# Optimization experiments

Hardware: AMD Instinct MI355X
Metric: run time of the kernel (lower is better)

Reference implementation:

```python
import jax, jax.numpy as jnp
import numpy as np

DIM = 2048
N_HEADS = 32
N_KV_HEADS = 8
HEAD_DIM = 64
REPEATS = N_HEADS // N_KV_HEADS
SLIDING_WINDOW = 1024
EPS = 1e-6
B, T = 2, 2048


def _alibi_slopes(n):
    # n_heads=32 is a power of 2
    r = 2.0 ** (-8.0 / n)
    return jnp.asarray([r ** i for i in range(n)], dtype=jnp.float32)


def _rms_norm(x, w, eps):
    # RMSNorm over the last (flattened heads*head_dim) axis
    var = jnp.mean(x * x, axis=-1, keepdims=True)
    return x * jax.lax.rsqrt(var + eps) * w


def setup_inputs() -> dict:
    key = jax.random.key(0)
    ks = jax.random.split(key, 6)
    s = 0.02
    return {
        "x": jax.random.normal(ks[0], (B, T, DIM), jnp.float32),
        "wq": jax.random.normal(ks[1], (N_HEADS * HEAD_DIM, DIM), jnp.float32) * s,
        "wk": jax.random.normal(ks[2], (N_KV_HEADS * HEAD_DIM, DIM), jnp.float32) * s,
        "wv": jax.random.normal(ks[3], (N_KV_HEADS * HEAD_DIM, DIM), jnp.float32) * s,
        "wo": jax.random.normal(ks[4], (DIM, N_HEADS * HEAD_DIM), jnp.float32) * s,
        "q_norm_w": jnp.ones((N_HEADS * HEAD_DIM,), jnp.float32),
        "k_norm_w": jnp.ones((N_KV_HEADS * HEAD_DIM,), jnp.float32),
    }


def reference(x, wq, wk, wv, wo, q_norm_w, k_norm_w):
    bsz, seqlen, _ = x.shape
    xq = _rms_norm(x @ wq.T, q_norm_w, EPS)
    xk = _rms_norm(x @ wk.T, k_norm_w, EPS)
    xv = x @ wv.T
    xq = xq.reshape(bsz, seqlen, N_HEADS, HEAD_DIM).transpose(0, 2, 1, 3)  # b h t d
    xk = xk.reshape(bsz, seqlen, N_KV_HEADS, HEAD_DIM).transpose(0, 2, 1, 3)
    xv = xv.reshape(bsz, seqlen, N_KV_HEADS, HEAD_DIM).transpose(0, 2, 1, 3)
    # GQA: repeat_interleave kv heads
    xk = jnp.repeat(xk, REPEATS, axis=1)
    xv = jnp.repeat(xv, REPEATS, axis=1)

    pos = jnp.arange(seqlen)
    dist = pos[None, :] - pos[:, None]                     # [t,s] = s - t (<=0 on causal side)
    slopes = _alibi_slopes(N_HEADS)
    alibi = slopes[:, None, None] * dist.astype(jnp.float32)  # [h,t,s]
    allowed = (dist <= 0) & (dist >= -SLIDING_WINDOW)      # causal + sliding window
    bias = jnp.where(allowed[None], alibi, -jnp.inf)       # [h,t,s]

    scale = 1.0 / jnp.sqrt(jnp.asarray(HEAD_DIM, jnp.float32))
    scores = jnp.einsum("bhtd,bhsd->bhts", xq, xk) * scale + bias[None]
    attn = jax.nn.softmax(scores, axis=-1)
    out = jnp.einsum("bhts,bhsd->bhtd", attn, xv)          # [b,h,t,d]
    out = out.transpose(0, 2, 1, 3).reshape(bsz, seqlen, N_HEADS * HEAD_DIM)
    return out @ wo.T
```

## Files before the change

kernel.cpp:

```cpp
#include <hip/hip_runtime.h>


typedef _Float16 f16;
typedef __attribute__((ext_vector_type(8))) _Float16 f16x8;
typedef __attribute__((ext_vector_type(4))) _Float16 f16x4;
typedef __attribute__((ext_vector_type(2))) _Float16 f16x2;
typedef __attribute__((ext_vector_type(4))) float f32x4;

#define T_ 2048
#define NH 32
#define NKV 8
#define HD 64
#define WINDOW 1024
#define EPS_ 1e-6f
#define LOG2E 1.44269504088896340736f
#define LDQKV 3072

__device__ inline void async16(void* lds, const void* g) {
  __builtin_amdgcn_global_load_lds(
      (const __attribute__((address_space(1))) unsigned int*)g,
      (__attribute__((address_space(3))) unsigned int*)lds, 16, 0, 0);
}

struct CvtArgs {
  const float* src[5];
  f16* dst[5];
  int n4[5];
};
__global__ __launch_bounds__(256) void cvt_multi(CvtArgs a) {
  const int seg = blockIdx.y;
  const float* in = a.src[seg];
  f16* out = a.dst[seg];
  const int n4 = a.n4[seg];
  for (int i = blockIdx.x * blockDim.x + threadIdx.x; i < n4;
       i += gridDim.x * blockDim.x) {
    float4 v = ((const float4*)in)[i];
    f16x4 o;
    o[0] = (f16)v.x; o[1] = (f16)v.y; o[2] = (f16)v.z; o[3] = (f16)v.w;
    ((f16x4*)out)[i] = o;
  }
}

#define DSRD(p, off) (*(const f16x8*)((p) + (off)))

__global__ __launch_bounds__(512, 1) void gemm_nt192(const f16* __restrict__ A,
                                                     const f16* __restrict__ B,
                                                     f16* __restrict__ C) {
  constexpr int K = 2048, ldc = 3072;
  extern __shared__ char smem[];
  f16* sA = (f16*)smem;
  f16* sB = (f16*)(smem + 65536);

  const int gx = gridDim.x;
  const int nwg = gx * gridDim.y;
  int bid = blockIdx.y * gx + blockIdx.x;
  bid = (bid & 7) * (nwg >> 3) + (bid >> 3);
  const int m0 = (bid / gx) * 256;
  const int n0 = (bid % gx) * 192;

  const int tid = threadIdx.x;
  const int lane = tid & 63;
  const int wave = tid >> 6;
  const int quad = lane >> 4, l16 = lane & 15;
  const int wm = wave >> 2, wn = wave & 3;

  const int srow = tid >> 3;
  const int sgr = (((tid & 7) ^ (srow & 7))) * 8;
  const f16* gA = A + (size_t)(m0 + srow) * K + sgr;
  const f16* gB = B + (size_t)(n0 + srow) * K + sgr;
  const size_t r64 = (size_t)64 * K;

  const char* cA = (const char*)sA;
  const char* cB = (const char*)sB;
  const int xm = (l16 & 7) << 4;
  const int xk0 = (quad * 16) ^ xm;
  const int xk1 = (64 + quad * 16) ^ xm;
  const int abase = (wm * 128 + l16) * 128;
  const int bbase = (wn * 48 + l16) * 128;

  f32x4 acc[8][3] = {};
  const int nt = K >> 6;

#pragma unroll
  for (int a = 0; a < 4; ++a)
    async16(sA + a * 4096 + tid * 8, gA + (size_t)a * r64);
#pragma unroll
  for (int rb = 0; rb < 3; ++rb)
    async16(sB + rb * 4096 + tid * 8, gB + (size_t)rb * r64);
  asm volatile("s_waitcnt vmcnt(0)" ::: "memory");
  __builtin_amdgcn_s_barrier();

  for (int t = 0; t < nt; ++t) {
    const int bufoA = (t & 1) << 15;
    const int bufoB = (t & 1) * 24576;
    f16* sAn = sA + (((t & 1) ^ 1) << 14);
    f16* sBn = sB + ((t & 1) ^ 1) * 12288;
    const bool st = (t + 1 < nt);
    const size_t gk = (size_t)(t + 1) * 64;

    f16x8 af[4], bf[3][2];

    auto ldA = [&](int mh, int xk) {
#pragma unroll
      for (int i = 0; i < 4; ++i)
        af[i] = DSRD(cA, bufoA + abase + mh * 8192 + i * 2048 + xk);
    };
    auto mm = [&](int mh, int kc) {
      __builtin_amdgcn_s_barrier();
      asm volatile("s_waitcnt lgkmcnt(0)" ::: "memory");
      __builtin_amdgcn_sched_barrier(0);
      __builtin_amdgcn_s_setprio(1);
#pragma unroll
      for (int i = 0; i < 4; ++i)
#pragma unroll
        for (int j = 0; j < 3; ++j)
          acc[mh * 4 + i][j] = __builtin_amdgcn_mfma_f32_16x16x32_f16(
              af[i], bf[j][kc], acc[mh * 4 + i][j], 0, 0, 0);
      __builtin_amdgcn_s_setprio(0);
    };

    ldA(0, xk0);
#pragma unroll
    for (int j = 0; j < 3; ++j) {
      bf[j][0] = DSRD(cB, bufoB + bbase + j * 2048 + xk0);
      bf[j][1] = DSRD(cB, bufoB + bbase + j * 2048 + xk1);
    }
    if (st) {
#pragma unroll
      for (int a = 0; a < 4; ++a)
        async16(sAn + a * 4096 + tid * 8, gA + a * r64 + gk);
    }
    mm(0, 0);
    __builtin_amdgcn_s_barrier();

    ldA(0, xk1);
    if (st) {
#pragma unroll
      for (int rb = 0; rb < 3; ++rb)
        async16(sBn + rb * 4096 + tid * 8, gB + rb * r64 + gk);
    }
    mm(0, 1);
    __builtin_amdgcn_s_barrier();

    ldA(1, xk0);
    mm(1, 0);
    __builtin_amdgcn_s_barrier();

    ldA(1, xk1);
    mm(1, 1);
    if (st) asm volatile("s_waitcnt vmcnt(0)" ::: "memory");
    __builtin_amdgcn_s_barrier();
  }

#pragma unroll
  for (int im = 0; im < 8; ++im) {
    const int row0 = m0 + wm * 128 + im * 16 + quad * 4;
#pragma unroll
    for (int j = 0; j < 3; ++j) {
      const int col = n0 + wn * 48 + j * 16 + l16;
#pragma unroll
      for (int r = 0; r < 4; ++r)
        C[(size_t)(row0 + r) * ldc + col] = (f16)acc[im][j][r];
    }
  }
}

template <int BN>
__global__ __launch_bounds__(512, 2) void gemm_nt8(const f16* __restrict__ A,
                                                   const f16* __restrict__ B,
                                                   void* __restrict__ C,
                                                   int M, int N, int K, int ldc,
                                                   int out_f32) {
  constexpr int WN = BN / 4;
  constexpr int JN = WN / 32;
  constexpr int RB = BN / 64;
  constexpr int BUFB = BN * 128;
  extern __shared__ char smem[];
  f16* sA = (f16*)smem;
  f16* sB = (f16*)(smem + 65536);

  const int gx = gridDim.x;
  const int nwg = gx * gridDim.y;
  int bid = blockIdx.y * gx + blockIdx.x;
  if (!(nwg & 7)) bid = (bid & 7) * (nwg >> 3) + (bid >> 3);
  const int m0 = (bid / gx) * 256;
  const int n0 = (bid % gx) * BN;

  const int tid = threadIdx.x;
  const int lane = tid & 63;
  const int wave = tid >> 6;
  const int quad = lane >> 4, l16 = lane & 15;
  const int wm = wave >> 2, wn = wave & 3;

  const int srow = tid >> 3;
  const int sgr = (((tid & 7) ^ (srow & 7))) * 8;
  const f16* gA = A + (size_t)(m0 + srow) * K + sgr;
  const f16* gB = B + (size_t)(n0 + srow) * K + sgr;
  const size_t r64 = (size_t)64 * K;

  const char* cA = (const char*)sA;
  const char* cB = (const char*)sB;
  const int xm = (l16 & 7) << 4;
  const int xk0 = (quad * 16) ^ xm;
  const int xk1 = (64 + quad * 16) ^ xm;
  const int abase = (wm * 128 + l16) * 128;
  const int bbase = (wn * WN + l16) * 128;

  f32x4 acc[8][2 * JN] = {};
  const int nt = K >> 6;

#pragma unroll
  for (int a = 0; a < 4; ++a)
    async16(sA + a * 4096 + tid * 8, gA + (size_t)a * r64);
#pragma unroll
  for (int rb = 0; rb < RB; ++rb)
    async16(sB + rb * 4096 + tid * 8, gB + (size_t)rb * r64);
  asm volatile("s_waitcnt vmcnt(0)" ::: "memory");
  __builtin_amdgcn_s_barrier();

  for (int t = 0; t < nt; ++t) {
    const int bufoA = (t & 1) << 15;
    const int bufoB = (t & 1) * BUFB;
    f16* sAn = sA + (((t & 1) ^ 1) << 14);
    f16* sBn = sB + ((t & 1) ^ 1) * (BUFB / 2);
    const bool st = (t + 1 < nt);
    const size_t gk = (size_t)(t + 1) * 64;

    f16x8 af[4][2], bf[JN][2];

    auto ldA = [&](int mh) {
#pragma unroll
      for (int i = 0; i < 4; ++i) {
        af[i][0] = DSRD(cA, bufoA + abase + mh * 8192 + i * 2048 + xk0);
        af[i][1] = DSRD(cA, bufoA + abase + mh * 8192 + i * 2048 + xk1);
      }
    };
    auto ldB = [&](int nh) {
#pragma unroll
      for (int j = 0; j < JN; ++j) {
        bf[j][0] = DSRD(cB, bufoB + bbase + nh * (WN / 2) * 128 + j * 2048 + xk0);
        bf[j][1] = DSRD(cB, bufoB + bbase + nh * (WN / 2) * 128 + j * 2048 + xk1);
      }
    };
    auto mm = [&](int mh, int nh) {
      __builtin_amdgcn_s_barrier();
      asm volatile("s_waitcnt lgkmcnt(0)" ::: "memory");
      __builtin_amdgcn_sched_barrier(0);
      __builtin_amdgcn_s_setprio(1);
#pragma unroll
      for (int i = 0; i < 4; ++i) {
#pragma unroll
        for (int j = 0; j < JN; ++j) {
          acc[mh * 4 + i][nh * JN + j] = __builtin_amdgcn_mfma_f32_16x16x32_f16(
              af[i][0], bf[j][0], acc[mh * 4 + i][nh * JN + j], 0, 0, 0);
          acc[mh * 4 + i][nh * JN + j] = __builtin_amdgcn_mfma_f32_16x16x32_f16(
              af[i][1], bf[j][1], acc[mh * 4 + i][nh * JN + j], 0, 0, 0);
        }
      }
      __builtin_amdgcn_s_setprio(0);
    };

    ldA(0); ldB(0);
    if (st) {
#pragma unroll
      for (int a = 0; a < 4; ++a)
        async16(sAn + a * 4096 + tid * 8, gA + a * r64 + gk);
#pragma unroll
      for (int rb = 0; rb < RB; ++rb)
        async16(sBn + rb * 4096 + tid * 8, gB + rb * r64 + gk);
    }
    mm(0, 0);
    __builtin_amdgcn_s_barrier();

    ldB(1);
    mm(0, 1);
    __builtin_amdgcn_s_barrier();

    ldA(1); ldB(0);
    mm(1, 0);
    __builtin_amdgcn_s_barrier();

    ldB(1);
    mm(1, 1);
    if (st) asm volatile("s_waitcnt vmcnt(0)" ::: "memory");
    __builtin_amdgcn_s_barrier();
  }

#pragma unroll
  for (int im = 0; im < 8; ++im) {
    const int row0 = m0 + wm * 128 + im * 16 + quad * 4;
#pragma unroll
    for (int jn = 0; jn < 2 * JN; ++jn) {
      const int col = n0 + wn * WN + jn * 16 + l16;
#pragma unroll
      for (int r = 0; r < 4; ++r) {
        const float v = acc[im][jn][r];
        if (out_f32) ((float*)C)[(size_t)(row0 + r) * ldc + col] = v;
        else         ((f16*)C)[(size_t)(row0 + r) * ldc + col] = (f16)v;
      }
    }
  }
}

__global__ __launch_bounds__(256) void rmsnorm2(f16* __restrict__ xqkv,
                                                const float* __restrict__ qw,
                                                const float* __restrict__ kw) {
  __shared__ float red[4];
  const int which = blockIdx.y;
  const int tid = threadIdx.x;

  auto block_sum = [&](float ss) -> float {
#pragma unroll
    for (int off = 32; off > 0; off >>= 1) ss += __shfl_down(ss, off);
    if ((tid & 63) == 0) red[tid >> 6] = ss;
    __syncthreads();
    return red[0] + red[1] + red[2] + red[3];
  };

  if (which == 0) {
    f16* p = xqkv + (size_t)blockIdx.x * LDQKV;
    f16x8 v = ((const f16x8*)p)[tid];
    float f[8];
    float ss = 0.f;
#pragma unroll
    for (int j = 0; j < 8; ++j) { f[j] = (float)v[j]; ss += f[j] * f[j]; }
    const float scale = rsqrtf(block_sum(ss) / 2048.0f + EPS_);
    const float4 w0 = ((const float4*)qw)[tid * 2];
    const float4 w1 = ((const float4*)qw)[tid * 2 + 1];
    f16x8 o;
    o[0] = (f16)(f[0] * scale * w0.x); o[1] = (f16)(f[1] * scale * w0.y);
    o[2] = (f16)(f[2] * scale * w0.z); o[3] = (f16)(f[3] * scale * w0.w);
    o[4] = (f16)(f[4] * scale * w1.x); o[5] = (f16)(f[5] * scale * w1.y);
    o[6] = (f16)(f[6] * scale * w1.z); o[7] = (f16)(f[7] * scale * w1.w);
    ((f16x8*)p)[tid] = o;
  } else {
    f16* p = xqkv + (size_t)blockIdx.x * LDQKV + 2048;
    f16x2 v = ((const f16x2*)p)[tid];
    const float f0 = (float)v[0], f1 = (float)v[1];
    const float scale = rsqrtf(block_sum(f0 * f0 + f1 * f1) / 512.0f + EPS_);
    const float2 w = ((const float2*)kw)[tid];
    f16x2 o;
    o[0] = (f16)(f0 * scale * w.x);
    o[1] = (f16)(f1 * scale * w.y);
    ((f16x2*)p)[tid] = o;
  }
}

__global__ __launch_bounds__(256) void kvfrag(const f16* __restrict__ xqkv,
                                              f16* __restrict__ Kf,
                                              f16* __restrict__ Vf) {
  __shared__ f16 Lk[64][72];
  __shared__ f16 Lv[64][72];
  const int kt = blockIdx.x;
  const int b = blockIdx.y >> 3, kh = blockIdx.y & 7;
  const int t0 = kt * 64;
  const int tid = threadIdx.x;
  const int r = tid >> 3, c = (tid & 7) * 8;
#pragma unroll
  for (int rp = 0; rp < 2; ++rp) {
    const int rr = r + rp * 32;
    const f16* src = xqkv + (size_t)(b * T_ + t0 + rr) * LDQKV + kh * 64 + c;
    *(f16x8*)(&Lk[rr][c]) = *(const f16x8*)(src + 2048);
    *(f16x8*)(&Lv[rr][c]) = *(const f16x8*)(src + 2560);
  }
  __syncthreads();
  const size_t obase = ((size_t)(b * 8 + kh) * 32 + kt) * 4096;
#pragma unroll
  for (int cc0 = 0; cc0 < 2; ++cc0) {
    const int cc = tid + cc0 * 256;
    const int nb = cc >> 7, kc = (cc >> 6) & 1, ln = cc & 63;
    const int qd = ln >> 4, s16 = ln & 15;
    *(f16x8*)(Kf + obase + cc * 8) = *(const f16x8*)(&Lk[nb * 16 + s16][kc * 32 + qd * 8]);
    f16x8 o;
#pragma unroll
    for (int j = 0; j < 8; ++j) o[j] = Lv[kc * 32 + qd * 8 + j][nb * 16 + s16];
    *(f16x8*)(Vf + obase + cc * 8) = o;
  }
}

__global__ __launch_bounds__(256, 8) void attn(const f16* __restrict__ Q,
                                               const f16* __restrict__ Kf,
                                               const f16* __restrict__ Vf,
                                               f16* __restrict__ O) {
  constexpr int LDW = 72;
  __shared__ f16 Qs[64 * LDW];
  __shared__ float Lx[4][16];

  const int qt = 31 - blockIdx.x;
  const int h = blockIdx.y, b = blockIdx.z;
  const int kh = h >> 2;
  const int q0 = qt * 64;
  const int tid = threadIdx.x;
  const int lane = tid & 63, wave = tid >> 6;
  const int quad = lane >> 4, l16 = lane & 15;
  const float scale2 = 0.125f * LOG2E;
  const float slope2 = exp2f(-0.25f * (float)h) * LOG2E;
  const float M2 = 10.0f;

  const int sr = tid >> 3, sc = (tid & 7) * 8;

#pragma unroll
  for (int rp = 0; rp < 2; ++rp) {
    const int rr = sr + rp * 32;
    *(f16x8*)(Qs + rr * LDW + sc) =
        *(const f16x8*)(Q + (size_t)(b * T_ + q0 + rr) * LDQKV + h * HD + sc);
  }
  __syncthreads();
  f16x8 qf[2];
#pragma unroll
  for (int kc = 0; kc < 2; ++kc)
    qf[kc] = *(const f16x8*)(Qs + (wave * 16 + l16) * LDW + kc * 32 + quad * 8);
  f16* Ps = Qs + wave * 16 * LDW;

  f32x4 o_acc[4] = {};
  float lsum = 0.f;

  const int kt_lo = (q0 >= WINDOW) ? ((q0 - WINDOW) >> 6) : 0;
  const int my_q = q0 + wave * 16 + l16;
  const f16* kfb = Kf + (size_t)(b * 8 + kh) * 131072 + lane * 8;
  const f16* vfb = Vf + (size_t)(b * 8 + kh) * 131072 + lane * 8;

  float sr4[4];
#pragma unroll
  for (int r = 0; r < 4; ++r) sr4[r] = slope2 * (float)r;
  float base = slope2 * (float)(kt_lo * 64 + quad * 4 - my_q) - M2;
  const float bstep = slope2 * 64.0f;
  const float b16 = slope2 * 16.0f;

  for (int kt = kt_lo; kt <= qt; ++kt) {
    const int k0 = kt * 64;
    const f16* kp = kfb + kt * 4096;
    const f16* vp = vfb + kt * 4096;
    const bool maskt = (kt == qt) || (q0 + 63 - k0 > WINDOW);

    float bnb = base;
#pragma unroll
    for (int nb = 0; nb < 4; ++nb) {
      f32x4 a = {0.f, 0.f, 0.f, 0.f};
#pragma unroll
      for (int kc = 0; kc < 2; ++kc) {
        const f16x8 kfr = *(const f16x8*)(kp + (nb * 2 + kc) * 512);
        a = __builtin_amdgcn_mfma_f32_16x16x32_f16(kfr, qf[kc], a, 0, 0, 0);
      }
      f16x4 pk;
#pragma unroll
      for (int r = 0; r < 4; ++r) {
        float v = fmaf(a[r], scale2, bnb + sr4[r]);
        if (maskt) {
          const int dist = k0 + nb * 16 + quad * 4 + r - my_q;
          if (dist > 0 || dist < -WINDOW) v = -1e30f;
        }
        const float p = __builtin_amdgcn_exp2f(v);
        lsum += p;
        pk[r] = (f16)p;
      }
      *(f16x4*)(Ps + l16 * LDW + nb * 16 + quad * 4) = pk;
      bnb += b16;
    }
    base += bstep;

#pragma unroll
    for (int nb = 0; nb < 4; ++nb) {
#pragma unroll
      for (int kc = 0; kc < 2; ++kc) {
        const f16x8 pa = *(const f16x8*)(Ps + l16 * LDW + kc * 32 + quad * 8);
        const f16x8 vb = *(const f16x8*)(vp + (nb * 2 + kc) * 512);
        o_acc[nb] = __builtin_amdgcn_mfma_f32_16x16x32_f16(pa, vb, o_acc[nb], 0, 0, 0);
      }
    }
  }

  lsum += __shfl_xor(lsum, 16);
  lsum += __shfl_xor(lsum, 32);
  if (quad == 0) Lx[wave][l16] = lsum;
  float rl[4];
#pragma unroll
  for (int r = 0; r < 4; ++r) rl[r] = 1.0f / Lx[wave][quad * 4 + r];

#pragma unroll
  for (int r = 0; r < 4; ++r) {
    const int q = q0 + wave * 16 + quad * 4 + r;
#pragma unroll
    for (int nb = 0; nb < 4; ++nb)
      O[(size_t)(b * T_ + q) * (NH * HD) + h * HD + nb * 16 + l16] =
          (f16)(o_acc[nb][r] * rl[r]);
  }
}

extern "C" void kernel_launch(void* const* d_in, const int* in_sizes, int n_in,
                              void* d_out, int out_size, void* d_ws, size_t ws_size,
                              hipStream_t stream) {
  const float* x  = (const float*)d_in[0];
  const float* wq = (const float*)d_in[1];
  const float* wk = (const float*)d_in[2];
  const float* wv = (const float*)d_in[3];
  const float* wo = (const float*)d_in[4];
  const float* qw = (const float*)d_in[5];
  const float* kw = (const float*)d_in[6];
  float* out = (float*)d_out;

  char* ws = (char*)d_ws;
  size_t off = 0;
  auto carve = [&](size_t bytes) -> char* {
    char* p = ws + off;
    off += (bytes + 255) & ~(size_t)255;
    return p;
  };
  f16* xh    = (f16*)carve((size_t)4096 * 2048 * 2);
  f16* wqkvh = (f16*)carve((size_t)3072 * 2048 * 2);
  f16* woh   = (f16*)carve((size_t)2048 * 2048 * 2);
  f16* xqkv  = (f16*)carve((size_t)4096 * 3072 * 2);
  f16* Kf = wqkvh;
  f16* Vf = wqkvh + (size_t)16 * 131072;
  f16* ao = xh;

  static bool attr_done = false;
  if (!attr_done) {
    (void)hipFuncSetAttribute((const void*)gemm_nt192,
                              hipFuncAttributeMaxDynamicSharedMemorySize,
                              114688);
    (void)hipFuncSetAttribute((const void*)gemm_nt8<128>,
                              hipFuncAttributeMaxDynamicSharedMemorySize,
                              98304);
    attr_done = true;
  }

  CvtArgs ca;
  ca.src[0] = x;  ca.dst[0] = xh;                            ca.n4[0] = (4096 * 2048) / 4;
  ca.src[1] = wq; ca.dst[1] = wqkvh;                         ca.n4[1] = (2048 * 2048) / 4;
  ca.src[2] = wk; ca.dst[2] = wqkvh + (size_t)2048 * 2048;   ca.n4[2] = (512 * 2048) / 4;
  ca.src[3] = wv; ca.dst[3] = wqkvh + (size_t)2560 * 2048;   ca.n4[3] = (512 * 2048) / 4;
  ca.src[4] = wo; ca.dst[4] = woh;                           ca.n4[4] = (2048 * 2048) / 4;
  cvt_multi<<<dim3(1024, 5), 256, 0, stream>>>(ca);

  gemm_nt192<<<dim3(16, 16), 512, 114688, stream>>>(xh, wqkvh, xqkv);
  rmsnorm2<<<dim3(4096, 2), 256, 0, stream>>>(xqkv, qw, kw);
  kvfrag<<<dim3(32, 16), 256, 0, stream>>>(xqkv, Kf, Vf);
  attn<<<dim3(32, 32, 2), 256, 0, stream>>>(xqkv, Kf, Vf, ao);
  gemm_nt8<128><<<dim3(16, 16), 512, 98304, stream>>>(ao, woh, out, 4096, 2048, 2048, 2048, 1);
}
```

Measured before the change: 305.7 us.

## Process 128 query rows per attention block to reuse K/V fragments

Each attention block now covers 128 query rows instead of 64, with each wave handling two 16-row sub-tiles that share every loaded K and V fragment. The aim is to halve the global K/V fragment traffic and the number of loads per MFMA. In exchange, register use per thread rises, launch bounds drop to 4 blocks per SM, the grid is half as large, and the tile spans more fully-masked key columns at the causal and window edges.

```diff
diff --git a/kernel.cpp b/kernel.cpp
--- a/kernel.cpp
+++ b/kernel.cpp
@@ -378,18 +378,18 @@
   }
 }
 
-__global__ __launch_bounds__(256, 8) void attn(const f16* __restrict__ Q,
+__global__ __launch_bounds__(256, 4) void attn(const f16* __restrict__ Q,
                                                const f16* __restrict__ Kf,
                                                const f16* __restrict__ Vf,
                                                f16* __restrict__ O) {
   constexpr int LDW = 72;
-  __shared__ f16 Qs[64 * LDW];
-  __shared__ float Lx[4][16];
-
-  const int qt = 31 - blockIdx.x;
+  __shared__ f16 Qs[128 * LDW];
+  __shared__ float Lx[4][2][16];
+
+  const int qt2 = 15 - blockIdx.x;
   const int h = blockIdx.y, b = blockIdx.z;
   const int kh = h >> 2;
-  const int q0 = qt * 64;
+  const int q0 = qt2 * 128;
   const int tid = threadIdx.x;
   const int lane = tid & 63, wave = tid >> 6;
   const int quad = lane >> 4, l16 = lane & 15;
@@ -400,90 +400,124 @@
   const int sr = tid >> 3, sc = (tid & 7) * 8;
 
 #pragma unroll
-  for (int rp = 0; rp < 2; ++rp) {
+  for (int rp = 0; rp < 4; ++rp) {
     const int rr = sr + rp * 32;
     *(f16x8*)(Qs + rr * LDW + sc) =
         *(const f16x8*)(Q + (size_t)(b * T_ + q0 + rr) * LDQKV + h * HD + sc);
   }
   __syncthreads();
-  f16x8 qf[2];
-#pragma unroll
-  for (int kc = 0; kc < 2; ++kc)
-    qf[kc] = *(const f16x8*)(Qs + (wave * 16 + l16) * LDW + kc * 32 + quad * 8);
-  f16* Ps = Qs + wave * 16 * LDW;
-
-  f32x4 o_acc[4] = {};
-  float lsum = 0.f;
+  f16x8 qa[2], qb[2];
+#pragma unroll
+  for (int kc = 0; kc < 2; ++kc) {
+    qa[kc] = *(const f16x8*)(Qs + (wave * 32 + l16) * LDW + kc * 32 + quad * 8);
+    qb[kc] = *(const f16x8*)(Qs + (wave * 32 + 16 + l16) * LDW + kc * 32 + quad * 8);
+  }
+  f16* PsA = Qs + (wave * 32) * LDW;
+  f16* PsB = Qs + (wave * 32 + 16) * LDW;
+
+  f32x4 o0[4] = {}, o1[4] = {};
+  float lsA = 0.f, lsB = 0.f;
 
   const int kt_lo = (q0 >= WINDOW) ? ((q0 - WINDOW) >> 6) : 0;
-  const int my_q = q0 + wave * 16 + l16;
+  const int kt_hi = (q0 + 127) >> 6;
+  const int gA0 = q0 + wave * 32;
+  const int gB0 = gA0 + 16;
+  const int qA = gA0 + l16;
+  const int qB = qA + 16;
   const f16* kfb = Kf + (size_t)(b * 8 + kh) * 131072 + lane * 8;
   const f16* vfb = Vf + (size_t)(b * 8 + kh) * 131072 + lane * 8;
 
   float sr4[4];
 #pragma unroll
   for (int r = 0; r < 4; ++r) sr4[r] = slope2 * (float)r;
-  float base = slope2 * (float)(kt_lo * 64 + quad * 4 - my_q) - M2;
+  float baseA = slope2 * (float)(kt_lo * 64 + quad * 4 - qA) - M2;
+  float baseB = slope2 * (float)(kt_lo * 64 + quad * 4 - qB) - M2;
   const float bstep = slope2 * 64.0f;
   const float b16 = slope2 * 16.0f;
 
-  for (int kt = kt_lo; kt <= qt; ++kt) {
+  for (int kt = kt_lo; kt <= kt_hi; ++kt) {
     const int k0 = kt * 64;
     const f16* kp = kfb + kt * 4096;
     const f16* vp = vfb + kt * 4096;
-    const bool maskt = (kt == qt) || (q0 + 63 - k0 > WINDOW);
-
-    float bnb = base;
+    const bool maskA = (k0 + 63 > gA0) || (k0 + WINDOW < gA0 + 15);
+    const bool maskB = (k0 + 63 > gB0) || (k0 + WINDOW < gB0 + 15);
+
+    float bnbA = baseA, bnbB = baseB;
 #pragma unroll
     for (int nb = 0; nb < 4; ++nb) {
+      const f16x8 k0f = *(const f16x8*)(kp + (nb * 2) * 512);
+      const f16x8 k1f = *(const f16x8*)(kp + (nb * 2 + 1) * 512);
       f32x4 a = {0.f, 0.f, 0.f, 0.f};
-#pragma unroll
-      for (int kc = 0; kc < 2; ++kc) {
-        const f16x8 kfr = *(const f16x8*)(kp + (nb * 2 + kc) * 512);
-        a = __builtin_amdgcn_mfma_f32_16x16x32_f16(kfr, qf[kc], a, 0, 0, 0);
+      a = __builtin_amdgcn_mfma_f32_16x16x32_f16(k0f, qa[0], a, 0, 0, 0);
+      a = __builtin_amdgcn_mfma_f32_16x16x32_f16(k1f, qa[1], a, 0, 0, 0);
+      f32x4 c = {0.f, 0.f, 0.f, 0.f};
+      c = __builtin_amdgcn_mfma_f32_16x16x32_f16(k0f, qb[0], c, 0, 0, 0);
+      c = __builtin_amdgcn_mfma_f32_16x16x32_f16(k1f, qb[1], c, 0, 0, 0);
+
+      f16x4 pkA, pkB;
+#pragma unroll
+      for (int r = 0; r < 4; ++r) {
+        const int key = k0 + nb * 16 + quad * 4 + r;
+        float vA = fmaf(a[r], scale2, bnbA + sr4[r]);
+        if (maskA) {
+          const int dist = key - qA;
+          if (dist > 0 || dist < -WINDOW) vA = -1e30f;
+        }
+        const float pA = __builtin_amdgcn_exp2f(vA);
+        lsA += pA;
+        pkA[r] = (f16)pA;
+        float vB = fmaf(c[r], scale2, bnbB + sr4[r]);
+        if (maskB) {
+          const int dist = key - qB;
+          if (dist > 0 || dist < -WINDOW) vB = -1e30f;
+        }
+        const float pB = __builtin_amdgcn_exp2f(vB);
+        lsB += pB;
+        pkB[r] = (f16)pB;
       }
-      f16x4 pk;
-#pragma unroll
-      for (int r = 0; r < 4; ++r) {
-        float v = fmaf(a[r], scale2, bnb + sr4[r]);
-        if (maskt) {
-          const int dist = k0 + nb * 16 + quad * 4 + r - my_q;
-          if (dist > 0 || dist < -WINDOW) v = -1e30f;
-        }
-        const float p = __builtin_amdgcn_exp2f(v);
-        lsum += p;
-        pk[r] = (f16)p;
-      }
-      *(f16x4*)(Ps + l16 * LDW + nb * 16 + quad * 4) = pk;
-      bnb += b16;
-    }
-    base += bstep;
-
+      *(f16x4*)(PsA + l16 * LDW + nb * 16 + quad * 4) = pkA;
+      *(f16x4*)(PsB + l16 * LDW + nb * 16 + quad * 4) = pkB;
+      bnbA += b16; bnbB += b16;
+    }
+    baseA += bstep; baseB += bstep;
+
+    const f16x8 paA0 = *(const f16x8*)(PsA + l16 * LDW + quad * 8);
+    const f16x8 paA1 = *(const f16x8*)(PsA + l16 * LDW + 32 + quad * 8);
+    const f16x8 paB0 = *(const f16x8*)(PsB + l16 * LDW + quad * 8);
+    const f16x8 paB1 = *(const f16x8*)(PsB + l16 * LDW + 32 + quad * 8);
 #pragma unroll
     for (int nb = 0; nb < 4; ++nb) {
-#pragma unroll
-      for (int kc = 0; kc < 2; ++kc) {
-        const f16x8 pa = *(const f16x8*)(Ps + l16 * LDW + kc * 32 + quad * 8);
-        const f16x8 vb = *(const f16x8*)(vp + (nb * 2 + kc) * 512);
-        o_acc[nb] = __builtin_amdgcn_mfma_f32_16x16x32_f16(pa, vb, o_acc[nb], 0, 0, 0);
-      }
-    }
-  }
-
-  lsum += __shfl_xor(lsum, 16);
-  lsum += __shfl_xor(lsum, 32);
-  if (quad == 0) Lx[wave][l16] = lsum;
-  float rl[4];
-#pragma unroll
-  for (int r = 0; r < 4; ++r) rl[r] = 1.0f / Lx[wave][quad * 4 + r];
-
+      const f16x8 v0 = *(const f16x8*)(vp + (nb * 2) * 512);
+      const f16x8 v1 = *(const f16x8*)(vp + (nb * 2 + 1) * 512);
+      o0[nb] = __builtin_amdgcn_mfma_f32_16x16x32_f16(paA0, v0, o0[nb], 0, 0, 0);
+      o0[nb] = __builtin_amdgcn_mfma_f32_16x16x32_f16(paA1, v1, o0[nb], 0, 0, 0);
+      o1[nb] = __builtin_amdgcn_mfma_f32_16x16x32_f16(paB0, v0, o1[nb], 0, 0, 0);
+      o1[nb] = __builtin_amdgcn_mfma_f32_16x16x32_f16(paB1, v1, o1[nb], 0, 0, 0);
+    }
+  }
+
+  lsA += __shfl_xor(lsA, 16);
+  lsA += __shfl_xor(lsA, 32);
+  lsB += __shfl_xor(lsB, 16);
+  lsB += __shfl_xor(lsB, 32);
+  if (quad == 0) { Lx[wave][0][l16] = lsA; Lx[wave][1][l16] = lsB; }
+  float rlA[4], rlB[4];
 #pragma unroll
   for (int r = 0; r < 4; ++r) {
-    const int q = q0 + wave * 16 + quad * 4 + r;
-#pragma unroll
-    for (int nb = 0; nb < 4; ++nb)
-      O[(size_t)(b * T_ + q) * (NH * HD) + h * HD + nb * 16 + l16] =
-          (f16)(o_acc[nb][r] * rl[r]);
+    rlA[r] = 1.0f / Lx[wave][0][quad * 4 + r];
+    rlB[r] = 1.0f / Lx[wave][1][quad * 4 + r];
+  }
+
+#pragma unroll
+  for (int r = 0; r < 4; ++r) {
+    const int qrA = q0 + wave * 32 + quad * 4 + r;
+#pragma unroll
+    for (int nb = 0; nb < 4; ++nb) {
+      O[(size_t)(b * T_ + qrA) * (NH * HD) + h * HD + nb * 16 + l16] =
+          (f16)(o0[nb][r] * rlA[r]);
+      O[(size_t)(b * T_ + qrA + 16) * (NH * HD) + h * HD + nb * 16 + l16] =
+          (f16)(o1[nb][r] * rlB[r]);
+    }
   }
 }
 
@@ -536,6 +570,6 @@
   gemm_nt192<<<dim3(16, 16), 512, 114688, stream>>>(xh, wqkvh, xqkv);
   rmsnorm2<<<dim3(4096, 2), 256, 0, stream>>>(xqkv, qw, kw);
   kvfrag<<<dim3(32, 16), 256, 0, stream>>>(xqkv, Kf, Vf);
-  attn<<<dim3(32, 32, 2), 256, 0, stream>>>(xqkv, Kf, Vf, ao);
+  attn<<<dim3(16, 32, 2), 256, 0, stream>>>(xqkv, Kf, Vf, ao);
   gemm_nt8<128><<<dim3(16, 16), 512, 98304, stream>>>(ao, woh, out, 4096, 2048, 2048, 2048, 1);
 }
```

Result: faster. 289.8 us (-5.2%).
